# Optimization experiments

Hardware: AMD Instinct MI355X
Metric: run time of the kernel (lower is better)

Reference implementation:

```python
import jax, jax.numpy as jnp
import numpy as np

N_EMBD = 1024
N_HEAD = 64

def setup_inputs() -> dict:
    key = jax.random.key(0)
    ks = jax.random.split(key, 7)
    B, T = 4, 4096
    x = jax.random.normal(ks[0], (B, T, N_EMBD), dtype=jnp.float32)
    # causal mask: True above the diagonal (masked positions)
    mask = jnp.triu(jnp.ones((T, T), dtype=bool), k=1)
    s = 1.0 / np.sqrt(N_EMBD)
    Wq = jax.random.normal(ks[1], (N_EMBD, N_HEAD), dtype=jnp.float32) * s
    bq = jnp.zeros((N_HEAD,), dtype=jnp.float32)
    Wk = jax.random.normal(ks[2], (N_EMBD, N_HEAD), dtype=jnp.float32) * s
    bk = jnp.zeros((N_HEAD,), dtype=jnp.float32)
    Wv = jax.random.normal(ks[3], (N_EMBD, N_HEAD), dtype=jnp.float32) * s
    bv = jnp.zeros((N_HEAD,), dtype=jnp.float32)
    return {"x": x, "mask": mask, "Wq": Wq, "bq": bq, "Wk": Wk, "bk": bk, "Wv": Wv, "bv": bv}

def reference(x, mask, Wq, bq, Wk, bk, Wv, bv):
    # x: [B,T,C], mask: [T,T] bool (True = masked)
    q = x @ Wq + bq            # [B,T,H]
    k = x @ Wk + bk            # [B,T,H]
    v = x @ Wv + bv            # [B,T,H]
    scale = 1.0 / jnp.sqrt(jnp.asarray(q.shape[-1], dtype=q.dtype))
    att = jnp.einsum('bth,bsh->bts', q, k) * scale   # [B,T,T]
    att = jnp.where(mask[None, :, :], -jnp.inf, att)
    att = jax.nn.softmax(att, axis=-1)
    # dropout omitted (eval mode / deterministic reference)
    return jnp.einsum('bts,bsh->bth', att, v)        # [B,T,H]
```

## Files before the change

### kernel.cpp

```cpp
#include <hip/hip_runtime.h>
#include <hip/hip_bf16.h>

#define BB 4
#define TT 4096
#define CC 1024
#define HH 64

#define QSCALE 0.18033688011112042f
#define FIXMAX2 23.083120654223414f

typedef __attribute__((ext_vector_type(8))) short short8;
typedef __attribute__((ext_vector_type(4))) float floatx4;

__device__ __forceinline__ ushort f2bf(float f) {
    union { float f; unsigned u; } a; a.f = f;
    const unsigned u = a.u;
    return (ushort)((u + 0x7fffu + ((u >> 16) & 1u)) >> 16);
}
__device__ __forceinline__ float bf2f(ushort h) {
    union { unsigned u; float f; } a; a.u = ((unsigned)h) << 16; return a.f;
}
__device__ __forceinline__ void load_lds16(const ushort* g, ushort* l) {
    __builtin_amdgcn_global_load_lds(
        (const __attribute__((address_space(1))) unsigned int*)g,
        (__attribute__((address_space(3))) unsigned int*)l, 16, 0, 0);
}

__global__ __launch_bounds__(256)
void wtrans_kernel(const float* __restrict__ Wq, const float* __restrict__ Wk,
                   const float* __restrict__ Wv, ushort* __restrict__ wT)
{
    __shared__ ushort tile[64 * 72];
    const int tid = threadIdx.x;
    const int mat = blockIdx.x >> 4, kt = blockIdx.x & 15;
    const float* W = (mat == 0) ? Wq : (mat == 1) ? Wk : Wv;
    #pragma unroll
    for (int it = 0; it < 16; ++it) {
        const int idx = it * 256 + tid;
        const int r = idx >> 6, c = idx & 63;
        tile[c * 72 + r] = f2bf(W[(size_t)(kt * 64 + r) * 64 + c]);
    }
    __syncthreads();
    #pragma unroll
    for (int it = 0; it < 16; ++it) {
        const int idx = it * 256 + tid;
        const int n = idx >> 6, kk = idx & 63;
        wT[((size_t)mat * 64 + n) * 1024 + kt * 64 + kk] = tile[n * 72 + kk];
    }
}

__global__ __launch_bounds__(256)
void qkv_mfma_kernel(const float* __restrict__ x, const ushort* __restrict__ wT,
                     const float* __restrict__ bq, const float* __restrict__ bk,
                     const float* __restrict__ bv,
                     ushort* __restrict__ q, ushort* __restrict__ k,
                     ushort* __restrict__ vT)
{
    __shared__ ushort xs [16 * 72];
    __shared__ ushort ws_[192 * 64];

    const int tid = threadIdx.x, w = tid >> 6, lane = tid & 63;
    const int m = lane & 15, quad = lane >> 4;
    const int row0 = blockIdx.x * 16;

    floatx4 acc[3];
    #pragma unroll
    for (int i = 0; i < 3; ++i) acc[i] = (floatx4){0.f, 0.f, 0.f, 0.f};

    const int lrow = lane >> 3;
    const int lg   = (lane & 7) ^ lrow;
    const ushort* gw = wT + (size_t)(w * 48 + lrow) * 1024 + lg * 8;
    ushort* lbase = ws_ + w * 6 * 512;

    const int xr = tid >> 4, xseg = tid & 15;

    const ushort* bfp[3][2];
    #pragma unroll
    for (int j = 0; j < 3; ++j)
        #pragma unroll
        for (int ks_ = 0; ks_ < 2; ++ks_)
            bfp[j][ks_] = ws_ + ((size_t)(w * 48 + j * 16 + m) * 8 +
                                 ((ks_ * 4 + quad) ^ (m & 7))) * 8;

    for (int kc = 0; kc < 16; ++kc) {
        const int k0 = kc * 64;
        __syncthreads();
        #pragma unroll
        for (int j = 0; j < 6; ++j)
            load_lds16(gw + (size_t)j * 8192 + k0, lbase + j * 512);
        {
            const float4 f0 = *(const float4*)(x + (size_t)(row0 + xr) * CC + k0 + xseg * 4);
            ushort4 p;
            p.x = f2bf(f0.x); p.y = f2bf(f0.y); p.z = f2bf(f0.z); p.w = f2bf(f0.w);
            *(ushort4*)(xs + xr * 72 + xseg * 4) = p;
        }
        __syncthreads();

        #pragma unroll
        for (int ks_ = 0; ks_ < 2; ++ks_) {
            const short8 a = *(const short8*)(xs + m * 72 + ks_ * 32 + quad * 8);
            #pragma unroll
            for (int j = 0; j < 3; ++j) {
                const short8 b_ = *(const short8*)bfp[j][ks_];
                acc[j] = __builtin_amdgcn_mfma_f32_16x16x32_bf16(a, b_, acc[j], 0, 0, 0);
            }
        }
    }

    const int gr0 = row0 + quad * 4;
    const int b_ = gr0 >> 12, t0 = gr0 & (TT - 1);
    #pragma unroll
    for (int j = 0; j < 3; ++j) {
        const int nt = w * 3 + j;
        const int mat = nt >> 2;
        const int c = (nt & 3) * 16 + m;
        const float bias = (mat == 0) ? bq[c] : (mat == 1) ? bk[c] : bv[c];
        if (mat == 0) {
            #pragma unroll
            for (int r = 0; r < 4; ++r)
                q[(size_t)(gr0 + r) * HH + c] = f2bf((acc[j][r] + bias) * QSCALE);
        } else if (mat == 1) {
            #pragma unroll
            for (int r = 0; r < 4; ++r)
                k[(size_t)(gr0 + r) * HH + c] = f2bf(acc[j][r] + bias);
        } else {
            ushort4 pv;
            pv.x = f2bf(acc[j][0] + bias); pv.y = f2bf(acc[j][1] + bias);
            pv.z = f2bf(acc[j][2] + bias); pv.w = f2bf(acc[j][3] + bias);
            *(ushort4*)(vT + ((size_t)b_ * HH + c) * TT + t0) = pv;
        }
    }
}

__global__ __launch_bounds__(256)
void attn_mfma_kernel(const ushort* __restrict__ q, const ushort* __restrict__ k,
                      const ushort* __restrict__ vT,
                      float* __restrict__ partL, ushort* __restrict__ partO)
{
    __shared__ ushort ks[64 * 72];
    __shared__ ushort vs[64 * 72];
    __shared__ ushort ps[4][16 * 72];

    const int tid = threadIdx.x, w = tid >> 6, lane = tid & 63;
    const int m = lane & 15, quad = lane >> 4;
    const int pid = blockIdx.x;
    const int job = pid >> 3, split = pid & 7;
    const int b = job >> 6, tile = job & 63;
    const int i0 = tile * 64;
    const int nch = tile + 1;
    const int lo = (nch * split) >> 3, hi = (nch * (split + 1)) >> 3;

    const size_t qrow = ((size_t)b * TT + i0 + w * 16 + m) * HH;
    const uint4 aq0u = *(const uint4*)(q + qrow + quad * 8);
    const uint4 aq1u = *(const uint4*)(q + qrow + 32 + quad * 8);
    const short8 aq0 = *(const short8*)&aq0u;
    const short8 aq1 = *(const short8*)&aq1u;

    float lrow[4] = {0.f, 0.f, 0.f, 0.f};
    floatx4 oacc[4];
    #pragma unroll
    for (int nt = 0; nt < 4; ++nt) oacc[nt] = (floatx4){0.f, 0.f, 0.f, 0.f};

    const int iq0 = i0 + w * 16;
    for (int ch = lo; ch < hi; ++ch) {
        const int s0 = ch * 64;
        __syncthreads();
        const size_t kb = ((size_t)b * TT + s0) * HH;
        #pragma unroll
        for (int it = 0; it < 2; ++it) {
            const int t2 = it * 256 + tid;
            const int r = t2 >> 3, seg = t2 & 7;
            *(uint4*)(ks + r * 72 + seg * 8) = *(const uint4*)(k + kb + (size_t)r * HH + seg * 8);
            *(uint4*)(vs + r * 72 + seg * 8) = *(const uint4*)(vT + ((size_t)b * HH + r) * TT + s0 + seg * 8);
        }
        __syncthreads();

        floatx4 sc[4];
        #pragma unroll
        for (int nt = 0; nt < 4; ++nt) {
            const short8 b0 = *(const short8*)(ks + (nt * 16 + m) * 72 + quad * 8);
            const short8 b1 = *(const short8*)(ks + (nt * 16 + m) * 72 + 32 + quad * 8);
            floatx4 s_ = (floatx4){0.f, 0.f, 0.f, 0.f};
            s_ = __builtin_amdgcn_mfma_f32_16x16x32_bf16(aq0, b0, s_, 0, 0, 0);
            s_ = __builtin_amdgcn_mfma_f32_16x16x32_bf16(aq1, b1, s_, 0, 0, 0);
            sc[nt] = s_;
        }

        const bool need_mask = (s0 + 63 > iq0);
        #pragma unroll
        for (int r = 0; r < 4; ++r) {
            float t0 = sc[0][r] - FIXMAX2;
            float t1 = sc[1][r] - FIXMAX2;
            float t2 = sc[2][r] - FIXMAX2;
            float t3 = sc[3][r] - FIXMAX2;
            if (need_mask) {
                const int dlim = iq0 + quad * 4 + r - s0 - m;
                if (0  > dlim) t0 = -1e30f;
                if (16 > dlim) t1 = -1e30f;
                if (32 > dlim) t2 = -1e30f;
                if (48 > dlim) t3 = -1e30f;
            }
            const float p0 = __builtin_amdgcn_exp2f(t0);
            const float p1 = __builtin_amdgcn_exp2f(t1);
            const float p2 = __builtin_amdgcn_exp2f(t2);
            const float p3 = __builtin_amdgcn_exp2f(t3);
            lrow[r] += (p0 + p1) + (p2 + p3);
            ushort* pr = ps[w] + (quad * 4 + r) * 72;
            pr[m]      = f2bf(p0);
            pr[16 + m] = f2bf(p1);
            pr[32 + m] = f2bf(p2);
            pr[48 + m] = f2bf(p3);
        }

        #pragma unroll
        for (int ks_ = 0; ks_ < 2; ++ks_) {
            const short8 ap = *(const short8*)(ps[w] + m * 72 + ks_ * 32 + quad * 8);
            #pragma unroll
            for (int nt = 0; nt < 4; ++nt) {
                const short8 bv_ = *(const short8*)(vs + (nt * 16 + m) * 72 + ks_ * 32 + quad * 8);
                oacc[nt] = __builtin_amdgcn_mfma_f32_16x16x32_bf16(ap, bv_, oacc[nt], 0, 0, 0);
            }
        }
    }

    #pragma unroll
    for (int r = 0; r < 4; ++r) {
        float s = lrow[r];
        s += __shfl_xor(s, 1); s += __shfl_xor(s, 2);
        s += __shfl_xor(s, 4); s += __shfl_xor(s, 8);
        lrow[r] = s;
    }
    if (m == 0) {
        #pragma unroll
        for (int r = 0; r < 4; ++r)
            partL[(size_t)pid * 64 + w * 16 + quad * 4 + r] = lrow[r];
    }
    ushort* po = partO + ((size_t)pid * 64 + w * 16) * 64;
    #pragma unroll
    for (int r = 0; r < 4; ++r) {
        const int row = quad * 4 + r;
        #pragma unroll
        for (int nt = 0; nt < 4; ++nt)
            po[row * 64 + nt * 16 + m] = f2bf(oacc[nt][r]);
    }
}

__global__ __launch_bounds__(256)
void attn_combine_kernel(const float* __restrict__ partL,
                         const ushort* __restrict__ partO, float* __restrict__ out)
{
    const int job = blockIdx.x;
    const int tid = threadIdx.x;
    const int row = tid >> 2, dq = tid & 3;

    float L = 0.f;
    #pragma unroll
    for (int s = 0; s < 8; ++s) L += partL[(size_t)(job * 8 + s) * 64 + row];
    const float inv = 1.f / L;

    float o[16];
    #pragma unroll
    for (int i = 0; i < 16; ++i) o[i] = 0.f;
    #pragma unroll
    for (int s = 0; s < 8; ++s) {
        const ushort* po = partO + (((size_t)(job * 8 + s) * 64 + row) * 64 + dq * 16);
        #pragma unroll
        for (int i2 = 0; i2 < 2; ++i2) {
            const ushort4 pa = *(const ushort4*)(po + i2 * 8);
            const ushort4 pb = *(const ushort4*)(po + i2 * 8 + 4);
            o[i2*8+0] += bf2f(pa.x); o[i2*8+1] += bf2f(pa.y);
            o[i2*8+2] += bf2f(pa.z); o[i2*8+3] += bf2f(pa.w);
            o[i2*8+4] += bf2f(pb.x); o[i2*8+5] += bf2f(pb.y);
            o[i2*8+6] += bf2f(pb.z); o[i2*8+7] += bf2f(pb.w);
        }
    }
    float4* dst = (float4*)(out + ((size_t)job * 64 + row) * 64 + dq * 16);
    #pragma unroll
    for (int i = 0; i < 4; ++i) {
        float4 v; v.x = o[i*4]*inv; v.y = o[i*4+1]*inv; v.z = o[i*4+2]*inv; v.w = o[i*4+3]*inv;
        dst[i] = v;
    }
}

extern "C" void kernel_launch(void* const* d_in, const int* in_sizes, int n_in,
                              void* d_out, int out_size, void* d_ws, size_t ws_size,
                              hipStream_t stream) {
    (void)in_sizes; (void)n_in; (void)out_size; (void)ws_size;
    const float* x  = (const float*)d_in[0];
    const float* Wq = (const float*)d_in[2];
    const float* bq = (const float*)d_in[3];
    const float* Wk = (const float*)d_in[4];
    const float* bk = (const float*)d_in[5];
    const float* Wv = (const float*)d_in[6];
    const float* bv = (const float*)d_in[7];
    float* out = (float*)d_out;

    char* ws = (char*)d_ws;
    ushort* wT    = (ushort*)ws;
    ushort* qb    = (ushort*)(ws + 393216);
    ushort* kb    = qb + (size_t)BB * TT * HH;
    ushort* vTb   = kb + (size_t)BB * TT * HH;
    float*  partL = (float*) (ws + 6684672);
    ushort* partO = (ushort*)(ws + 7208960);

    wtrans_kernel   <<<48, 256, 0, stream>>>(Wq, Wk, Wv, wT);
    qkv_mfma_kernel <<<(BB * TT) / 16, 256, 0, stream>>>(x, wT, bq, bk, bv, qb, kb, vTb);
    attn_mfma_kernel<<<BB * 64 * 8, 256, 0, stream>>>(qb, kb, vTb, partL, partO);
    attn_combine_kernel<<<BB * 64, 256, 0, stream>>>(partL, partO, out);
}
```

Before: 206.8 us.

## Double-buffer QKV projection LDS tiles and process 32 rows per block

The QKV projection kernel now double-buffers both the x tile and the weight tile in LDS, issuing the next chunk's global loads before the current chunk's MFMAs and leaving one barrier per iteration. Each block now handles 32 rows instead of 16, so every weight fragment read from LDS feeds twice as many MFMAs and weight traffic per row halves. In exchange LDS use roughly doubles, register pressure rises, and the grid has half as many blocks, which can lower occupancy.

Result: faster. 200.3 us (-3.1%).

```diff
diff --git a/kernel.cpp b/kernel.cpp
--- a/kernel.cpp
+++ b/kernel.cpp
@@ -10,6 +10,7 @@
 #define FIXMAX2 23.083120654223414f
 
 typedef __attribute__((ext_vector_type(8))) short short8;
+typedef __attribute__((ext_vector_type(8))) ushort ushortx8;
 typedef __attribute__((ext_vector_type(4))) float floatx4;
 
 __device__ __forceinline__ ushort f2bf(float f) {
@@ -56,78 +57,110 @@
                      ushort* __restrict__ q, ushort* __restrict__ k,
                      ushort* __restrict__ vT)
 {
-    __shared__ ushort xs [16 * 72];
-    __shared__ ushort ws_[192 * 64];
+    __shared__ ushort xs [2][32 * 72];
+    __shared__ ushort ws_[2][192 * 64];
 
     const int tid = threadIdx.x, w = tid >> 6, lane = tid & 63;
     const int m = lane & 15, quad = lane >> 4;
-    const int row0 = blockIdx.x * 16;
-
-    floatx4 acc[3];
-    #pragma unroll
-    for (int i = 0; i < 3; ++i) acc[i] = (floatx4){0.f, 0.f, 0.f, 0.f};
+    const int row0 = blockIdx.x * 32;
+
+    floatx4 acc[2][3];
+    #pragma unroll
+    for (int mi = 0; mi < 2; ++mi)
+        #pragma unroll
+        for (int j = 0; j < 3; ++j) acc[mi][j] = (floatx4){0.f, 0.f, 0.f, 0.f};
 
     const int lrow = lane >> 3;
     const int lg   = (lane & 7) ^ lrow;
     const ushort* gw = wT + (size_t)(w * 48 + lrow) * 1024 + lg * 8;
-    ushort* lbase = ws_ + w * 6 * 512;
-
-    const int xr = tid >> 4, xseg = tid & 15;
-
-    const ushort* bfp[3][2];
+
+    const int xr = tid >> 3, xseg = tid & 7;
+    const float* gx = x + (size_t)(row0 + xr) * CC + xseg * 8;
+
+    int bslot[3][2];
     #pragma unroll
     for (int j = 0; j < 3; ++j)
         #pragma unroll
         for (int ks_ = 0; ks_ < 2; ++ks_)
-            bfp[j][ks_] = ws_ + ((size_t)(w * 48 + j * 16 + m) * 8 +
-                                 ((ks_ * 4 + quad) ^ (m & 7))) * 8;
+            bslot[j][ks_] = ((w * 48 + j * 16 + m) * 8 +
+                             ((ks_ * 4 + quad) ^ (m & 7))) * 8;
+
+    {
+        const float4 xa = *(const float4*)(gx);
+        const float4 xb = *(const float4*)(gx + 4);
+        #pragma unroll
+        for (int j = 0; j < 6; ++j)
+            load_lds16(gw + (size_t)j * 8192, &ws_[0][w * 3072 + j * 512]);
+        ushortx8 p;
+        p[0] = f2bf(xa.x); p[1] = f2bf(xa.y); p[2] = f2bf(xa.z); p[3] = f2bf(xa.w);
+        p[4] = f2bf(xb.x); p[5] = f2bf(xb.y); p[6] = f2bf(xb.z); p[7] = f2bf(xb.w);
+        *(ushortx8*)(&xs[0][xr * 72 + xseg * 8]) = p;
+    }
+    __syncthreads();
 
     for (int kc = 0; kc < 16; ++kc) {
-        const int k0 = kc * 64;
-        __syncthreads();
-        #pragma unroll
-        for (int j = 0; j < 6; ++j)
-            load_lds16(gw + (size_t)j * 8192 + k0, lbase + j * 512);
-        {
-            const float4 f0 = *(const float4*)(x + (size_t)(row0 + xr) * CC + k0 + xseg * 4);
-            ushort4 p;
-            p.x = f2bf(f0.x); p.y = f2bf(f0.y); p.z = f2bf(f0.z); p.w = f2bf(f0.w);
-            *(ushort4*)(xs + xr * 72 + xseg * 4) = p;
-        }
-        __syncthreads();
-
-        #pragma unroll
-        for (int ks_ = 0; ks_ < 2; ++ks_) {
-            const short8 a = *(const short8*)(xs + m * 72 + ks_ * 32 + quad * 8);
+        const int cur = kc & 1;
+        float4 na, nb;
+        if (kc < 15) {
+            const int k0n = (kc + 1) * 64;
+            na = *(const float4*)(gx + k0n);
+            nb = *(const float4*)(gx + k0n + 4);
+            #pragma unroll
+            for (int j = 0; j < 6; ++j)
+                load_lds16(gw + (size_t)j * 8192 + k0n, &ws_[cur ^ 1][w * 3072 + j * 512]);
+        }
+        const ushort* xb_ = xs[cur];
+        const ushort* wb_ = ws_[cur];
+        short8 bfr[3][2];
+        #pragma unroll
+        for (int j = 0; j < 3; ++j)
+            #pragma unroll
+            for (int ks_ = 0; ks_ < 2; ++ks_)
+                bfr[j][ks_] = *(const short8*)(wb_ + bslot[j][ks_]);
+        #pragma unroll
+        for (int mi = 0; mi < 2; ++mi) {
+            const short8 a0 = *(const short8*)(xb_ + (mi * 16 + m) * 72 + quad * 8);
+            const short8 a1 = *(const short8*)(xb_ + (mi * 16 + m) * 72 + 32 + quad * 8);
             #pragma unroll
             for (int j = 0; j < 3; ++j) {
-                const short8 b_ = *(const short8*)bfp[j][ks_];
-                acc[j] = __builtin_amdgcn_mfma_f32_16x16x32_bf16(a, b_, acc[j], 0, 0, 0);
+                acc[mi][j] = __builtin_amdgcn_mfma_f32_16x16x32_bf16(a0, bfr[j][0], acc[mi][j], 0, 0, 0);
+                acc[mi][j] = __builtin_amdgcn_mfma_f32_16x16x32_bf16(a1, bfr[j][1], acc[mi][j], 0, 0, 0);
             }
         }
-    }
-
-    const int gr0 = row0 + quad * 4;
-    const int b_ = gr0 >> 12, t0 = gr0 & (TT - 1);
+        if (kc < 15) {
+            ushortx8 p;
+            p[0] = f2bf(na.x); p[1] = f2bf(na.y); p[2] = f2bf(na.z); p[3] = f2bf(na.w);
+            p[4] = f2bf(nb.x); p[5] = f2bf(nb.y); p[6] = f2bf(nb.z); p[7] = f2bf(nb.w);
+            *(ushortx8*)(&xs[cur ^ 1][xr * 72 + xseg * 8]) = p;
+        }
+        __syncthreads();
+    }
+
+    const int b_ = row0 >> 12, tb = row0 & (TT - 1);
     #pragma unroll
     for (int j = 0; j < 3; ++j) {
         const int nt = w * 3 + j;
         const int mat = nt >> 2;
         const int c = (nt & 3) * 16 + m;
         const float bias = (mat == 0) ? bq[c] : (mat == 1) ? bk[c] : bv[c];
-        if (mat == 0) {
-            #pragma unroll
-            for (int r = 0; r < 4; ++r)
-                q[(size_t)(gr0 + r) * HH + c] = f2bf((acc[j][r] + bias) * QSCALE);
-        } else if (mat == 1) {
-            #pragma unroll
-            for (int r = 0; r < 4; ++r)
-                k[(size_t)(gr0 + r) * HH + c] = f2bf(acc[j][r] + bias);
-        } else {
-            ushort4 pv;
-            pv.x = f2bf(acc[j][0] + bias); pv.y = f2bf(acc[j][1] + bias);
-            pv.z = f2bf(acc[j][2] + bias); pv.w = f2bf(acc[j][3] + bias);
-            *(ushort4*)(vT + ((size_t)b_ * HH + c) * TT + t0) = pv;
+        #pragma unroll
+        for (int mi = 0; mi < 2; ++mi) {
+            const int gr0 = row0 + mi * 16 + quad * 4;
+            if (mat == 0) {
+                #pragma unroll
+                for (int r = 0; r < 4; ++r)
+                    q[(size_t)(gr0 + r) * HH + c] = f2bf((acc[mi][j][r] + bias) * QSCALE);
+            } else if (mat == 1) {
+                #pragma unroll
+                for (int r = 0; r < 4; ++r)
+                    k[(size_t)(gr0 + r) * HH + c] = f2bf(acc[mi][j][r] + bias);
+            } else {
+                ushort4 pv;
+                pv.x = f2bf(acc[mi][j][0] + bias); pv.y = f2bf(acc[mi][j][1] + bias);
+                pv.z = f2bf(acc[mi][j][2] + bias); pv.w = f2bf(acc[mi][j][3] + bias);
+                const int t0 = tb + mi * 16 + quad * 4;
+                *(ushort4*)(vT + ((size_t)b_ * HH + c) * TT + t0) = pv;
+            }
         }
     }
 }
@@ -304,7 +337,7 @@
     ushort* partO = (ushort*)(ws + 7208960);
 
     wtrans_kernel   <<<48, 256, 0, stream>>>(Wq, Wk, Wv, wT);
-    qkv_mfma_kernel <<<(BB * TT) / 16, 256, 0, stream>>>(x, wT, bq, bk, bv, qb, kb, vTb);
+    qkv_mfma_kernel <<<(BB * TT) / 32, 256, 0, stream>>>(x, wT, bq, bk, bv, qb, kb, vTb);
     attn_mfma_kernel<<<BB * 64 * 8, 256, 0, stream>>>(qb, kb, vTb, partL, partO);
     attn_combine_kernel<<<BB * 64, 256, 0, stream>>>(partL, partO, out);
 }
```
